# Kernel optimization log

Hardware: AMD Instinct MI355X
Metric: run time of the kernel (lower is better)

Reference implementation:

```python
import jax, jax.numpy as jnp
import numpy as np
from jax import lax


def _layernorm(x, scale, bias, eps=1e-5):
    m = x.mean(-1, keepdims=True)
    v = x.var(-1, keepdims=True)
    return (x - m) / jnp.sqrt(v + eps) * scale + bias


def setup_inputs() -> dict:
    key = jax.random.key(0)
    d = 21                      # code distance
    S = d * d - 1               # 440 tokens
    g = d + 1                   # 22x22 grid
    D, H, F, L, B = 256, 8, 512, 6, 64
    ks = jax.random.split(key, 24)
    w = 0.02
    idx = np.arange(S)
    scatter_positions = jnp.asarray(np.stack([idx // g, idx % g], axis=1), dtype=jnp.int64)
    inp = {
        'x': jax.random.randint(ks[0], (B, S), 0, 2).astype(jnp.int64),
        'scatter_positions': scatter_positions,
        'event_emb': w * jax.random.normal(ks[1], (2, D), jnp.float32),
        'pos_x': w * jax.random.normal(ks[2], (2 * d + 1, D), jnp.float32),
        'pos_y': w * jax.random.normal(ks[3], (2 * d + 1, D), jnp.float32),
        'stab_emb': w * jax.random.normal(ks[4], (2, D), jnp.float32),
        'tok_x': jax.random.randint(ks[5], (S,), 0, 2 * d + 1).astype(jnp.int64),
        'tok_y': jax.random.randint(ks[6], (S,), 0, 2 * d + 1).astype(jnp.int64),
        'tok_stab': jax.random.randint(ks[7], (S,), 0, 2).astype(jnp.int64),
        'attn_bias': w * jax.random.normal(ks[8], (S, S), jnp.float32),
        'Wqkv': w * jax.random.normal(ks[9], (L, 3 * D, D), jnp.float32),
        'bqkv': jnp.zeros((L, 3 * D), jnp.float32),
        'Wo': w * jax.random.normal(ks[10], (L, D, D), jnp.float32),
        'bo': jnp.zeros((L, D), jnp.float32),
        'W1': w * jax.random.normal(ks[11], (L, F, D), jnp.float32),
        'b1': jnp.zeros((L, F), jnp.float32),
        'W2': w * jax.random.normal(ks[12], (L, D, F), jnp.float32),
        'b2': jnp.zeros((L, D), jnp.float32),
        'ln1_s': jnp.ones((L, D), jnp.float32),
        'ln1_b': jnp.zeros((L, D), jnp.float32),
        'ln2_s': jnp.ones((L, D), jnp.float32),
        'ln2_b': jnp.zeros((L, D), jnp.float32),
        'cw1': w * jax.random.normal(ks[13], (L, D, D // H, 3, 3), jnp.float32),
        'cb1': jnp.zeros((L, D), jnp.float32),
        'cw2': w * jax.random.normal(ks[14], (L, D, D // H, 3, 3), jnp.float32),
        'cb2': jnp.zeros((L, D), jnp.float32),
        'cw3': w * jax.random.normal(ks[15], (L, D, D // H, 3, 3), jnp.float32),
        'cb3': jnp.zeros((L, D), jnp.float32),
    }
    return inp


def _forward(x, scatter_positions, event_emb, pos_x, pos_y, stab_emb, tok_x, tok_y,
             tok_stab, attn_bias, Wqkv, bqkv, Wo, bo, W1, b1, W2, b2,
             ln1_s, ln1_b, ln2_s, ln2_b, cw1, cb1, cw2, cb2, cw3, cb3):
    B, S = x.shape
    D = event_emb.shape[1]
    L = Wqkv.shape[0]
    H = D // cw1.shape[2]           # groups = n_heads
    dh = D // H
    g = int(np.sqrt(S + 1)) + 1     # (d+1) grid side
    rows = scatter_positions[:, 0]
    cols = scatter_positions[:, 1]

    # 2D positional encoding gathers + event embedding
    pos = pos_x[tok_x] + pos_y[tok_y] + stab_emb[tok_stab]   # [S, D]
    h = event_emb[x] + pos[None]                             # [B, S, D]

    scale = 1.0 / np.sqrt(dh).astype(np.float32)

    def conv(xg, wgt, b, dil):
        y = lax.conv_general_dilated(
            xg, wgt, window_strides=(1, 1), padding=[(dil, dil), (dil, dil)],
            rhs_dilation=(dil, dil), feature_group_count=H,
            dimension_numbers=('NCHW', 'OIHW', 'NCHW'))
        return jax.nn.relu(y + b[None, :, None, None])

    for l in range(L):
        # --- bias-MHA: QK^T * scale + learned relative bias, softmax, V ---
        qkv = jnp.einsum('bsd,ed->bse', h, Wqkv[l]) + bqkv[l]
        q, k, v = jnp.split(qkv, 3, axis=-1)
        q = q.reshape(B, S, H, dh)
        k = k.reshape(B, S, H, dh)
        v = v.reshape(B, S, H, dh)
        scores = jnp.einsum('bqhd,bkhd->bhqk', q, k) * scale + attn_bias[None, None]
        p = jax.nn.softmax(scores, axis=-1)
        o = jnp.einsum('bhqk,bkhd->bqhd', p, v).reshape(B, S, D)
        a = jnp.einsum('bsd,ed->bse', o, Wo[l]) + bo[l]
        h = _layernorm(h + a, ln1_s[l], ln1_b[l])
        # --- FFN (post-norm, ReLU) ---
        ff = jax.nn.relu(jnp.einsum('bsd,fd->bsf', h, W1[l]) + b1[l])
        ff = jnp.einsum('bsf,df->bsd', ff, W2[l]) + b2[l]
        h = _layernorm(h + ff, ln2_s[l], ln2_b[l])
        # --- scatter to 2D grid, grouped dilated convs, collect back ---
        grid = jnp.zeros((B, g, g, D), h.dtype).at[:, rows, cols].set(h)
        xg = grid.transpose(0, 3, 1, 2)                       # NCHW
        xg = 0.5 * (xg + conv(xg, cw1[l], cb1[l], 1)
                       + conv(xg, cw2[l], cb2[l], 2)
                       + conv(xg, cw3[l], cb3[l], 3))
        h = xg.transpose(0, 2, 3, 1)[:, rows, cols]           # collect_from_2d
    return h


def reference(x, scatter_positions, event_emb, pos_x, pos_y, stab_emb, tok_x, tok_y,
              tok_stab, attn_bias, Wqkv, bqkv, Wo, bo, W1, b1, W2, b2,
              ln1_s, ln1_b, ln2_s, ln2_b, cw1, cb1, cw2, cb2, cw3, cb3):
    return _forward(x, scatter_positions, event_emb, pos_x, pos_y, stab_emb, tok_x,
                    tok_y, tok_stab, attn_bias, Wqkv, bqkv, Wo, bo, W1, b1, W2, b2,
                    ln1_s, ln1_b, ln2_s, ln2_b, cw1, cb1, cw2, cb2, cw3, cb3)
```

## Files before the change

### kernel.cpp

```cpp
#include <hip/hip_runtime.h>
#include <hip/hip_bf16.h>

#define NB 64
#define S 440
#define D 256
#define H 8
#define DH 32
#define F 512
#define NL 6
#define G 22
#define NT (NB*S)
#define QBLK 224
#define QT2 2
#define PADK 456
#define CSTR 40

typedef __hip_bfloat16 bf16;
typedef unsigned short u16;
typedef __bf16 bf16x8 __attribute__((ext_vector_type(8)));
typedef float f32x4 __attribute__((ext_vector_type(4)));

#define MAGIC_BF16 0x3F803F80u

__device__ __align__(16) u16 g_abT[(S / 4) * S * 4];
#define WOFF_QKV 0
#define WOFF_WO  (NL*3*D*D)
#define WOFF_W1  (WOFF_WO + NL*D*D)
#define WOFF_W2  (WOFF_W1 + NL*F*D)
__device__ __align__(16) u16 g_wlin[WOFF_W2 + NL*D*F];
#define CVSTRIDE ((size_t)NL * 9 * 8 * 1024)
__device__ __align__(16) u16 g_cwt[3 * CVSTRIDE];
__device__ __align__(16) u16 g_qkvb[(size_t)NT * 768];
__device__ __align__(16) u16 g_obuf[(size_t)NT * D];
__device__ __align__(16) u16 g_acb [(size_t)NT * D];
__device__ __align__(16) u16 g_hbb [(size_t)NT * D];

static __device__ __forceinline__ float bf2f(bf16 x) { return __bfloat162float(x); }
static __device__ __forceinline__ float u2f(u16 u) {
  union { unsigned int i; float f; } t; t.i = ((unsigned int)u) << 16; return t.f;
}
static __device__ __forceinline__ float i2f(unsigned v) {
  union { unsigned u; float f; } t; t.u = v; return t.f;
}
static __device__ __forceinline__ u16 f2u(float f) {
  bf16 h = __float2bfloat16(f);
  return *(u16*)&h;
}
static __device__ __forceinline__ unsigned cvt_pk(float lo, float hi) {
  unsigned r;
  asm("v_cvt_pk_bf16_f32 %0, %1, %2" : "=v"(r) : "v"(lo), "v"(hi));
  return r;
}
static __device__ __forceinline__ float ldT(const void* p, size_t i, bool bfm) {
  return bfm ? u2f(((const u16*)p)[i]) : ((const float*)p)[i];
}
static __device__ __forceinline__ bf16x8 as_bf16x8(uint4 v) {
  union { uint4 u; bf16x8 b; } t; t.u = v; return t.b;
}
static __device__ __forceinline__ void gload_lds16(const u16* g, u16* l) {
  __builtin_amdgcn_global_load_lds(
      (const __attribute__((address_space(1))) void*)g,
      (__attribute__((address_space(3))) void*)l, 16, 0, 0);
}
static __device__ __forceinline__ const u16* selbuf(const void* ext, int sel) {
  return sel == 0 ? (const u16*)ext : sel == 1 ? g_hbb : sel == 2 ? g_qkvb : g_obuf;
}

__global__ void __launch_bounds__(256) cvt_conv(
    const void* __restrict__ src, int which, const unsigned* __restrict__ probe)
{
  bool bfm = (*probe == MAGIC_BF16);
  int n = NL * D * DH * 9;
  int i = blockIdx.x * 256 + threadIdx.x;
  if (i >= n) return;
  int kk = i % 9;
  int ic = (i / 9) % DH;
  int oc = (i / 288) % D;
  int l  = i / 73728;
  int g = oc >> 5, oc32 = oc & 31;
  u16 v;
  if (bfm) v = ((const u16*)src)[i];
  else     v = f2u(((const float*)src)[i]);
  g_cwt[(size_t)which * CVSTRIDE + (((size_t)l * 9 + kk) * 8 + g) * 1024 + oc32 * 32 + ic] = v;
}

__global__ void __launch_bounds__(256) cvt_lin(
    const void* __restrict__ src, size_t dstoff, int n,
    const unsigned* __restrict__ probe)
{
  bool bfm = (*probe == MAGIC_BF16);
  int i = blockIdx.x * 256 + threadIdx.x;
  if (i >= n) return;
  g_wlin[dstoff + i] = bfm ? ((const u16*)src)[i] : f2u(((const float*)src)[i]);
}

__global__ void __launch_bounds__(256) cvt_bias(
    const void* __restrict__ ab, const unsigned* __restrict__ probe)
{
  bool bfm = (*probe == MAGIC_BF16);
  int i = blockIdx.x * 256 + threadIdx.x;
  if (i >= (S / 4) * S * 4) return;
  int j = i & 3;
  int t = i >> 2;
  int q = t % S;
  int k4 = t / S;
  int k = k4 * 4 + j;
  float v = ldT(ab, (size_t)q * S + k, bfm) * 1.4426950408889634f;
  g_abT[i] = f2u(v);
}

__global__ void __launch_bounds__(256) embed_kernel(
    const int* __restrict__ x, const void* __restrict__ event_emb,
    const void* __restrict__ pos_x, const void* __restrict__ pos_y,
    const void* __restrict__ stab_emb, const int* __restrict__ tok_x,
    const int* __restrict__ tok_y, const int* __restrict__ tok_stab,
    bf16* __restrict__ h, const unsigned* __restrict__ probe)
{
  bool bfm = (*probe == MAGIC_BF16);
  int d = threadIdx.x;
#pragma unroll
  for (int r = 0; r < 4; ++r) {
    int t = blockIdx.x * 4 + r;
    int b = t / S, s = t - b * S;
    float v = ldT(event_emb, (size_t)x[b * S + s] * D + d, bfm)
            + ldT(pos_x, (size_t)tok_x[s] * D + d, bfm)
            + ldT(pos_y, (size_t)tok_y[s] * D + d, bfm)
            + ldT(stab_emb, (size_t)tok_stab[s] * D + d, bfm);
    h[(size_t)t * D + d] = __float2bfloat16(v);
  }
}

template <int RELU>
__global__ void __launch_bounds__(256) gemm_mfma(
    const void* __restrict__ Aext, int asel, size_t woff,
    const void* __restrict__ bias, size_t boff, int csel,
    int M, int N, int K, const unsigned* __restrict__ probe)
{
  bool bfm = (*probe == MAGIC_BF16);
  __shared__ u16 As[2][128][32];
  __shared__ u16 Ws[2][128][32];
  int tid = threadIdx.x;
  int bn = blockIdx.x, bm = blockIdx.y;
  int lane = tid & 63, w = tid >> 6;
  int wm = (w >> 1) * 64, wn = (w & 1) * 64;
  int qd = lane >> 4, ln16 = lane & 15;
  f32x4 zero4 = {0.f, 0.f, 0.f, 0.f};
  f32x4 acc[4][4];
#pragma unroll
  for (int i = 0; i < 4; ++i)
#pragma unroll
    for (int j = 0; j < 4; ++j) acc[i][j] = zero4;

  const u16* Au = selbuf(Aext, asel);
  u16* Cu = (csel == 0) ? g_qkvb : g_acb;
  const u16* Wu = g_wlin + woff;
  int srow = w * 32 + (lane >> 2);
  int skc  = (lane & 3) << 3;
  size_t abase = (size_t)(bm * 128 + srow) * K + skc;
  size_t wbase = (size_t)(bn * 128 + srow) * K + skc;

  gload_lds16(Au + abase,                   &As[0][w * 32][0]);
  gload_lds16(Au + abase + (size_t)16 * K,  &As[0][w * 32 + 16][0]);
  gload_lds16(Wu + wbase,                   &Ws[0][w * 32][0]);
  gload_lds16(Wu + wbase + (size_t)16 * K,  &Ws[0][w * 32 + 16][0]);

  int cur = 0;
  for (int k0 = 0; k0 < K; k0 += 32) {
    __syncthreads();
    if (k0 + 32 < K) {
      int nb = cur ^ 1;
      gload_lds16(Au + abase + k0 + 32,                  &As[nb][w * 32][0]);
      gload_lds16(Au + abase + (size_t)16 * K + k0 + 32, &As[nb][w * 32 + 16][0]);
      gload_lds16(Wu + wbase + k0 + 32,                  &Ws[nb][w * 32][0]);
      gload_lds16(Wu + wbase + (size_t)16 * K + k0 + 32, &Ws[nb][w * 32 + 16][0]);
    }
    bf16x8 af[4], bfr[4];
#pragma unroll
    for (int t = 0; t < 4; ++t) {
      af[t]  = *(const bf16x8*)&As[cur][wm + t * 16 + ln16][qd * 8];
      bfr[t] = *(const bf16x8*)&Ws[cur][wn + t * 16 + ln16][qd * 8];
    }
#pragma unroll
    for (int mt = 0; mt < 4; ++mt)
#pragma unroll
      for (int nt = 0; nt < 4; ++nt)
        acc[mt][nt] = __builtin_amdgcn_mfma_f32_16x16x32_bf16(af[mt], bfr[nt], acc[mt][nt], 0, 0, 0);
    cur ^= 1;
  }
#pragma unroll
  for (int nt = 0; nt < 4; ++nt) {
    int gcol = bn * 128 + wn + nt * 16 + ln16;
    float bv = ldT(bias, boff + gcol, bfm);
#pragma unroll
    for (int mt = 0; mt < 4; ++mt) {
#pragma unroll
      for (int r = 0; r < 4; ++r) {
        int grow = bm * 128 + wm + mt * 16 + qd * 4 + r;
        float v = acc[mt][nt][r] + bv;
        if (RELU) v = fmaxf(v, 0.f);
        Cu[(size_t)grow * N + gcol] = f2u(v);
      }
    }
  }
}

__global__ void __launch_bounds__(448) attn_mfma()
{
  __shared__ u16 VT[32 * PADK];
  int tid = threadIdx.x;
  int blk = blockIdx.x;
  int qt = (blk >> 3) & 1;
  int bh = ((blk >> 4) << 3) | (blk & 7);
  int hh = bh % H;
  int b  = bh / H;
  int lane = tid & 63, w = tid >> 6;
  int qd = lane >> 4, ln16 = lane & 15;
  const u16* qkvu = g_qkvb;

  unsigned* VT32 = (unsigned*)VT;
#pragma unroll
  for (int i = 0; i < 2; ++i) {
    int slot = tid + i * 448;
    int rp = slot >> 2, kc = slot & 3;
    int r0 = rp * 2;
    uint4 va = make_uint4(0, 0, 0, 0), vb = make_uint4(0, 0, 0, 0);
    if (r0 < S)     va = *(const uint4*)&qkvu[((size_t)(b * S + r0)) * 768 + 512 + hh * DH + kc * 8];
    if (r0 + 1 < S) vb = *(const uint4*)&qkvu[((size_t)(b * S + r0 + 1)) * 768 + 512 + hh * DH + kc * 8];
    unsigned aw[4] = {va.x, va.y, va.z, va.w};
    unsigned bw[4] = {vb.x, vb.y, vb.z, vb.w};
#pragma unroll
    for (int jj = 0; jj < 4; ++jj) {
      int d = kc * 8 + jj * 2;
      VT32[(size_t)(d    ) * (PADK / 2) + rp] = (aw[jj] & 0xffffu) | ((bw[jj] & 0xffffu) << 16);
      VT32[(size_t)(d + 1) * (PADK / 2) + rp] = (aw[jj] >> 16)     | ((bw[jj] >> 16) << 16);
    }
  }

  int q0 = qt * QBLK + w * 32;
  int qaA = q0 + ln16;      if (qaA >= S) qaA = S - 1;
  int qaB = q0 + 16 + ln16; if (qaB >= S) qaB = S - 1;
  bf16x8 afA = *(const bf16x8*)&qkvu[((size_t)(b * S + qaA)) * 768 + hh * DH + qd * 8];
  bf16x8 afB = *(const bf16x8*)&qkvu[((size_t)(b * S + qaB)) * 768 + hh * DH + qd * 8];
  __syncthreads();

  int kperm = ((ln16 >> 2) << 3) + (ln16 & 3);
  auto kload = [&](int ks_, int half) -> uint4 {
    int tok = ks_ * 32 + kperm + half * 4;
    if (tok >= S) tok = S - 1;
    return *(const uint4*)&qkvu[((size_t)(b * S + tok)) * 768 + 256 + hh * DH + qd * 8];
  };
  uint4 kn0 = kload(0, 0), kn1 = kload(0, 1);

  float lsA = 0.f, lsB = 0.f;
  f32x4 zero4 = {0.f, 0.f, 0.f, 0.f};
  f32x4 oa0A = zero4, oa1A = zero4;
  f32x4 oa0B = zero4, oa1B = zero4;
  const float SC2 = 0.17677669529663689f * 1.4426950408889634f;

  auto bias4 = [&](uint2 wv, float* o) {
    o[0] = i2f(wv.x << 16); o[1] = i2f(wv.x & 0xffff0000u);
    o[2] = i2f(wv.y << 16); o[3] = i2f(wv.y & 0xffff0000u);
  };

  auto body = [&](int ks, bool masked) {
    int k4a = ks * 8 + 2 * qd;
    int k4b = k4a + 1;
    if (masked) { if (k4a > 109) k4a = 109; if (k4b > 109) k4b = 109; }
    uint2 bwaA = *(const uint2*)&g_abT[((size_t)k4a * S + qaA) * 4];
    uint2 bwbA = *(const uint2*)&g_abT[((size_t)k4b * S + qaA) * 4];
    uint2 bwaB = *(const uint2*)&g_abT[((size_t)k4a * S + qaB) * 4];
    uint2 bwbB = *(const uint2*)&g_abT[((size_t)k4b * S + qaB) * 4];
    bf16x8 kf0 = as_bf16x8(kn0), kf1 = as_bf16x8(kn1);
    if (!masked) { kn0 = kload(ks + 1, 0); kn1 = kload(ks + 1, 1); }
    f32x4 s0A = __builtin_amdgcn_mfma_f32_16x16x32_bf16(kf0, afA, zero4, 0, 0, 0);
    f32x4 s1A = __builtin_amdgcn_mfma_f32_16x16x32_bf16(kf1, afA, zero4, 0, 0, 0);
    f32x4 s0B = __builtin_amdgcn_mfma_f32_16x16x32_bf16(kf0, afB, zero4, 0, 0, 0);
    f32x4 s1B = __builtin_amdgcn_mfma_f32_16x16x32_bf16(kf1, afB, zero4, 0, 0, 0);
    float bAA[4], bBA[4], bAB[4], bBB[4];
    bias4(bwaA, bAA); bias4(bwbA, bBA); bias4(bwaB, bAB); bias4(bwbB, bBB);
    float pA[8], pB[8];
    if (!masked) {
#pragma unroll
      for (int r = 0; r < 4; ++r) {
        pA[r]     = exp2f(fminf(fmaf(s0A[r], SC2, bAA[r]), 80.f));
        pA[4 + r] = exp2f(fminf(fmaf(s1A[r], SC2, bBA[r]), 80.f));
        pB[r]     = exp2f(fminf(fmaf(s0B[r], SC2, bAB[r]), 80.f));
        pB[4 + r] = exp2f(fminf(fmaf(s1B[r], SC2, bBB[r]), 80.f));
      }
    } else {
      int c0 = ks * 32 + qd * 8;
#pragma unroll
      for (int r = 0; r < 4; ++r) {
        bool m0 = (c0 + r < S), m1 = (c0 + 4 + r < S);
        pA[r]     = exp2f(m0 ? fminf(fmaf(s0A[r], SC2, bAA[r]), 80.f) : -1e30f);
        pA[4 + r] = exp2f(m1 ? fminf(fmaf(s1A[r], SC2, bBA[r]), 80.f) : -1e30f);
        pB[r]     = exp2f(m0 ? fminf(fmaf(s0B[r], SC2, bAB[r]), 80.f) : -1e30f);
        pB[4 + r] = exp2f(m1 ? fminf(fmaf(s1B[r], SC2, bBB[r]), 80.f) : -1e30f);
      }
    }
    lsA += ((pA[0] + pA[1]) + (pA[2] + pA[3])) + ((pA[4] + pA[5]) + (pA[6] + pA[7]));
    lsB += ((pB[0] + pB[1]) + (pB[2] + pB[3])) + ((pB[4] + pB[5]) + (pB[6] + pB[7]));
    bf16x8 pfA = as_bf16x8(make_uint4(
        cvt_pk(pA[0], pA[1]), cvt_pk(pA[2], pA[3]),
        cvt_pk(pA[4], pA[5]), cvt_pk(pA[6], pA[7])));
    bf16x8 pfB = as_bf16x8(make_uint4(
        cvt_pk(pB[0], pB[1]), cvt_pk(pB[2], pB[3]),
        cvt_pk(pB[4], pB[5]), cvt_pk(pB[6], pB[7])));
    int kb = ks * 32;
    bf16x8 vf0 = *(const bf16x8*)&VT[(size_t)ln16 * PADK + kb + qd * 8];
    bf16x8 vf1 = *(const bf16x8*)&VT[(size_t)(16 + ln16) * PADK + kb + qd * 8];
    oa0A = __builtin_amdgcn_mfma_f32_16x16x32_bf16(vf0, pfA, oa0A, 0, 0, 0);
    oa1A = __builtin_amdgcn_mfma_f32_16x16x32_bf16(vf1, pfA, oa1A, 0, 0, 0);
    oa0B = __builtin_amdgcn_mfma_f32_16x16x32_bf16(vf0, pfB, oa0B, 0, 0, 0);
    oa1B = __builtin_amdgcn_mfma_f32_16x16x32_bf16(vf1, pfB, oa1B, 0, 0, 0);
  };

  for (int ks = 0; ks < 13; ++ks) body(ks, false);
  body(13, true);

  lsA += __shfl_xor(lsA, 16, 64);
  lsA += __shfl_xor(lsA, 32, 64);
  lsB += __shfl_xor(lsB, 16, 64);
  lsB += __shfl_xor(lsB, 32, 64);
  float invA = 1.0f / lsA, invB = 1.0f / lsB;
  int qA = q0 + ln16, qB = q0 + 16 + ln16;
  if (qA < S) {
    u16* op = g_obuf + ((size_t)(b * S + qA)) * D + hh * DH;
    *(uint2*)&op[qd * 4] = make_uint2(
        cvt_pk(oa0A[0] * invA, oa0A[1] * invA),
        cvt_pk(oa0A[2] * invA, oa0A[3] * invA));
    *(uint2*)&op[16 + qd * 4] = make_uint2(
        cvt_pk(oa1A[0] * invA, oa1A[1] * invA),
        cvt_pk(oa1A[2] * invA, oa1A[3] * invA));
  }
  if (qB < S) {
    u16* op = g_obuf + ((size_t)(b * S + qB)) * D + hh * DH;
    *(uint2*)&op[qd * 4] = make_uint2(
        cvt_pk(oa0B[0] * invB, oa0B[1] * invB),
        cvt_pk(oa0B[2] * invB, oa0B[3] * invB));
    *(uint2*)&op[16 + qd * 4] = make_uint2(
        cvt_pk(oa1B[0] * invB, oa1B[1] * invB),
        cvt_pk(oa1B[2] * invB, oa1B[3] * invB));
  }
}

__global__ void __launch_bounds__(256) add_ln_kernel(
    void* __restrict__ hext, int hsel,
    const void* __restrict__ sc, size_t soff,
    const void* __restrict__ bi, size_t boff2,
    const unsigned* __restrict__ probe)
{
  bool bfm = (*probe == MAGIC_BF16);
  int wv = threadIdx.x >> 6, lane = threadIdx.x & 63;
  size_t row = (size_t)blockIdx.x * 4 + wv;
  u16* hp = (hsel ? g_hbb : (u16*)hext) + row * D;
  const u16* ap = g_acb + row * D;
  uint2 hv = *(const uint2*)&hp[lane * 4];
  uint2 av = *(const uint2*)&ap[lane * 4];
  float v0 = u2f((u16)(hv.x & 0xffffu)) + u2f((u16)(av.x & 0xffffu));
  float v1 = u2f((u16)(hv.x >> 16))     + u2f((u16)(av.x >> 16));
  float v2 = u2f((u16)(hv.y & 0xffffu)) + u2f((u16)(av.y & 0xffffu));
  float v3 = u2f((u16)(hv.y >> 16))     + u2f((u16)(av.y >> 16));
  float s = (v0 + v1) + (v2 + v3);
#pragma unroll
  for (int o = 1; o <= 32; o <<= 1) s += __shfl_xor(s, o, 64);
  float mean = s * (1.0f / D);
  float c0 = v0 - mean, c1 = v1 - mean, c2 = v2 - mean, c3 = v3 - mean;
  float vs = (c0 * c0 + c1 * c1) + (c2 * c2 + c3 * c3);
#pragma unroll
  for (int o = 1; o <= 32; o <<= 1) vs += __shfl_xor(vs, o, 64);
  float r = rsqrtf(vs * (1.0f / D) + 1e-5f);
  int d = lane * 4;
  float o0 = c0 * r * ldT(sc, soff + d,     bfm) + ldT(bi, boff2 + d,     bfm);
  float o1 = c1 * r * ldT(sc, soff + d + 1, bfm) + ldT(bi, boff2 + d + 1, bfm);
  float o2 = c2 * r * ldT(sc, soff + d + 2, bfm) + ldT(bi, boff2 + d + 2, bfm);
  float o3 = c3 * r * ldT(sc, soff + d + 3, bfm) + ldT(bi, boff2 + d + 3, bfm);
  *(uint2*)&hp[lane * 4] = make_uint2(cvt_pk(o0, o1), cvt_pk(o2, o3));
}

__global__ void __launch_bounds__(256) conv_mfma(
    const void* __restrict__ hin_ext, int hinsel,
    const void* __restrict__ cb1, const void* __restrict__ cb2,
    const void* __restrict__ cb3, size_t cboff,
    void* __restrict__ hout_ext, int houtsel, int l, int final_,
    const unsigned* __restrict__ probe)
{
  bool bfm = (*probe == MAGIC_BF16);
  __shared__ u16 X[17 * 28 * CSTR];
  int half = blockIdx.x, g = blockIdx.y, b = blockIdx.z;
  int tid = threadIdx.x;
  int rb = half ? 7 : -3;
  const u16* hin = selbuf(hin_ext, hinsel);

  for (int i = tid; i < 17 * 28 * CSTR / 8; i += 256)
    *(uint4*)&X[i * 8] = make_uint4(0, 0, 0, 0);
  __syncthreads();
  int rv0 = half ? 7 : 0;
  int nrow = half ? 13 : 14;
  for (int i = tid; i < nrow * 22 * 4; i += 256) {
    int tk = i >> 2, ch = i & 3;
    int r = rv0 + tk / 22, c = tk % 22;
    uint4 v = *(const uint4*)&hin[((size_t)(b * S + r * 22 + c)) * D + g * 32 + ch * 8];
    *(uint4*)&X[(((r - rb) * 28) + (c + 3)) * CSTR + ch * 8] = v;
  }
  __syncthreads();

  int lane = tid & 63, w = tid >> 6;
  int qd = lane >> 4, ln16 = lane & 15;
  int nt = w & 1;
  int mq = w >> 1;
  int t_base = half * 224 + mq * 112;
  int oc_l = nt * 16 + ln16;

  int aoff[7];
#pragma unroll
  for (int mt = 0; mt < 7; ++mt) {
    int t = t_base + mt * 16 + ln16;
    if (t > S - 1) t = S - 1;
    int r = t / 22, c = t - r * 22;
    aoff[mt] = (((r - rb) * 28) + (c + 3)) * CSTR;
  }
  f32x4 fin[7];
#pragma unroll
  for (int mt = 0; mt < 7; ++mt) {
#pragma unroll
    for (int r4 = 0; r4 < 4; ++r4) {
      int t = t_base + mt * 16 + qd * 4 + r4;
      if (t > S - 1) t = S - 1;
      int r = t / 22, c = t - r * 22;
      fin[mt][r4] = u2f(X[(((r - rb) * 28) + (c + 3)) * CSTR + oc_l]);
    }
  }

  f32x4 zero4 = {0.f, 0.f, 0.f, 0.f};
  const void* cbs[3] = {cb1, cb2, cb3};
#pragma unroll
  for (int cv = 0; cv < 3; ++cv) {
    int dil = cv + 1;
    f32x4 acc[7];
#pragma unroll
    for (int mt = 0; mt < 7; ++mt) acc[mt] = zero4;
    const u16* wt = g_cwt + ((size_t)cv * NL + l) * (9 * 8 * 1024);
#pragma unroll
    for (int kk = 0; kk < 9; ++kk) {
      int off = ((kk / 3 - 1) * 28 + (kk % 3 - 1)) * dil * CSTR;
      bf16x8 bfrag = *(const bf16x8*)&wt[((size_t)kk * 8 + g) * 1024 + oc_l * 32 + qd * 8];
#pragma unroll
      for (int mt = 0; mt < 7; ++mt) {
        bf16x8 a = *(const bf16x8*)&X[aoff[mt] + off + qd * 8];
        acc[mt] = __builtin_amdgcn_mfma_f32_16x16x32_bf16(a, bfrag, acc[mt], 0, 0, 0);
      }
    }
    float bv = ldT(cbs[cv], cboff + g * 32 + oc_l, bfm);
#pragma unroll
    for (int mt = 0; mt < 7; ++mt)
#pragma unroll
      for (int r4 = 0; r4 < 4; ++r4)
        fin[mt][r4] += fmaxf(acc[mt][r4] + bv, 0.f);
  }

#pragma unroll
  for (int mt = 0; mt < 7; ++mt)
#pragma unroll
    for (int r4 = 0; r4 < 4; ++r4) {
      int t = t_base + mt * 16 + qd * 4 + r4;
      if (t < S) {
        float outv = 0.5f * fin[mt][r4];
        size_t oi = ((size_t)(b * S + t)) * D + g * 32 + oc_l;
        if (final_ && !bfm) ((float*)hout_ext)[oi] = outv;
        else {
          u16* ho = houtsel ? g_hbb : (u16*)hout_ext;
          ho[oi] = f2u(outv);
        }
      }
    }
}

extern "C" void kernel_launch(void* const* d_in, const int* in_sizes, int n_in,
                              void* d_out, int out_size, void* d_ws, size_t ws_size,
                              hipStream_t stream)
{
  const int*  x         = (const int*)d_in[0];
  const void* event_emb = d_in[2];
  const void* pos_x     = d_in[3];
  const void* pos_y     = d_in[4];
  const void* stab_emb  = d_in[5];
  const int*  tok_x     = (const int*)d_in[6];
  const int*  tok_y     = (const int*)d_in[7];
  const int*  tok_stab  = (const int*)d_in[8];
  const void* attn_bias = d_in[9];
  const void* Wqkv      = d_in[10];
  const void* bqkv      = d_in[11];
  const void* Wo        = d_in[12];
  const void* bo        = d_in[13];
  const void* W1        = d_in[14];
  const void* b1        = d_in[15];
  const void* W2        = d_in[16];
  const void* b2        = d_in[17];
  const void* ln1_s     = d_in[18];
  const void* ln1_b     = d_in[19];
  const void* ln2_s     = d_in[20];
  const void* ln2_b     = d_in[21];
  const void* cw1       = d_in[22];
  const void* cb1       = d_in[23];
  const void* cw2       = d_in[24];
  const void* cb2       = d_in[25];
  const void* cw3       = d_in[26];
  const void* cb3       = d_in[27];
  (void)in_sizes; (void)n_in; (void)out_size; (void)d_ws; (void)ws_size;
  const unsigned* probe = (const unsigned*)ln1_s;

  int ncv = NL * D * DH * 9;
  cvt_conv<<<(ncv + 255)/256, 256, 0, stream>>>(cw1, 0, probe);
  cvt_conv<<<(ncv + 255)/256, 256, 0, stream>>>(cw2, 1, probe);
  cvt_conv<<<(ncv + 255)/256, 256, 0, stream>>>(cw3, 2, probe);
  cvt_bias<<<((S/4)*S*4 + 255)/256, 256, 0, stream>>>(attn_bias, probe);
  cvt_lin<<<(NL*3*D*D + 255)/256, 256, 0, stream>>>(Wqkv, WOFF_QKV, NL*3*D*D, probe);
  cvt_lin<<<(NL*D*D   + 255)/256, 256, 0, stream>>>(Wo,   WOFF_WO,  NL*D*D,   probe);
  cvt_lin<<<(NL*F*D   + 255)/256, 256, 0, stream>>>(W1,   WOFF_W1,  NL*F*D,   probe);
  cvt_lin<<<(NL*D*F   + 255)/256, 256, 0, stream>>>(W2,   WOFF_W2,  NL*D*F,   probe);

  bf16* hout_ = (bf16*)d_out;
  embed_kernel<<<NT/4, 256, 0, stream>>>(x, event_emb, pos_x, pos_y, stab_emb,
                                         tok_x, tok_y, tok_stab, hout_, probe);

  for (int l = 0; l < NL; ++l) {
    int hs = l & 1;
    int fin = (l == NL - 1) ? 1 : 0;
    gemm_mfma<0><<<dim3(6, NT/128), 256, 0, stream>>>(
        hout_, hs, (size_t)WOFF_QKV + (size_t)l*3*D*D, bqkv, (size_t)l*3*D, 0,
        NT, 3*D, D, probe);
    attn_mfma<<<NB*H*QT2, 448, 0, stream>>>();
    gemm_mfma<0><<<dim3(2, NT/128), 256, 0, stream>>>(
        hout_, 3, (size_t)WOFF_WO + (size_t)l*D*D, bo, (size_t)l*D, 1,
        NT, D, D, probe);
    add_ln_kernel<<<NT/4, 256, 0, stream>>>(hout_, hs, ln1_s, (size_t)l*D, ln1_b, (size_t)l*D, probe);
    gemm_mfma<1><<<dim3(4, NT/128), 256, 0, stream>>>(
        hout_, hs, (size_t)WOFF_W1 + (size_t)l*F*D, b1, (size_t)l*F, 0,
        NT, F, D, probe);
    gemm_mfma<0><<<dim3(2, NT/128), 256, 0, stream>>>(
        hout_, 2, (size_t)WOFF_W2 + (size_t)l*D*F, b2, (size_t)l*D, 1,
        NT, D, F, probe);
    add_ln_kernel<<<NT/4, 256, 0, stream>>>(hout_, hs, ln2_s, (size_t)l*D, ln2_b, (size_t)l*D, probe);
    conv_mfma<<<dim3(2, 8, NB), 256, 0, stream>>>(
        hout_, hs, cb1, cb2, cb3, (size_t)l*D, hout_, hs ^ 1, l, fin, probe);
  }
}
```

Measured before the change: 1.422 ms.

## Fuse output-projection and FFN-down GEMMs with residual add and LayerNorm

Adds a gemm_ln kernel in which each block computes a full 128x256 output row tile, adds bias and the residual, and applies LayerNorm using a cross-wave reduction through shared memory. It replaces the Wo and W2 GEMMs plus their separate add_ln kernels, removing the bf16 round trip of the intermediate activations and two launches per layer. Grid parallelism drops from 2x220 blocks to 220 larger blocks of 512 threads. Variance is now computed as E[x^2]-mean^2, which is less numerically stable than the previous two-pass form.

```diff
diff --git a/kernel.cpp b/kernel.cpp
--- a/kernel.cpp
+++ b/kernel.cpp
@@ -202,6 +202,125 @@
       }
     }
   }
+}
+
+__global__ void __launch_bounds__(512) gemm_ln(
+    const void* __restrict__ Aext, int asel, size_t woff,
+    const void* __restrict__ bias, size_t boff,
+    void* __restrict__ hext, int hsel,
+    const void* __restrict__ sc, size_t soff,
+    const void* __restrict__ bi, size_t boff2,
+    int K, const unsigned* __restrict__ probe)
+{
+  bool bfm = (*probe == MAGIC_BF16);
+  __shared__ u16 As[2][128][32];
+  __shared__ u16 Ws[2][256][32];
+  __shared__ float redS[4][128];
+  __shared__ float redQ[4][128];
+  int tid = threadIdx.x;
+  int bm = blockIdx.x;
+  int lane = tid & 63, w = tid >> 6;
+  int wm = (w >> 2) * 64, wn = (w & 3) * 64;
+  int qd = lane >> 4, ln16 = lane & 15;
+  f32x4 zero4 = {0.f, 0.f, 0.f, 0.f};
+  f32x4 acc[4][4];
+#pragma unroll
+  for (int i = 0; i < 4; ++i)
+#pragma unroll
+    for (int j = 0; j < 4; ++j) acc[i][j] = zero4;
+
+  const u16* Au = selbuf(Aext, asel);
+  u16* hp = hsel ? g_hbb : (u16*)hext;
+  const u16* Wu = g_wlin + woff;
+  int arow = w * 16 + (lane >> 2);
+  int wrow = w * 32 + (lane >> 2);
+  int skc  = (lane & 3) << 3;
+  size_t abase = (size_t)(bm * 128 + arow) * K + skc;
+  size_t wbase = (size_t)wrow * K + skc;
+
+  gload_lds16(Au + abase,                  &As[0][w * 16][0]);
+  gload_lds16(Wu + wbase,                  &Ws[0][w * 32][0]);
+  gload_lds16(Wu + wbase + (size_t)16 * K, &Ws[0][w * 32 + 16][0]);
+
+  int cur = 0;
+  for (int k0 = 0; k0 < K; k0 += 32) {
+    __syncthreads();
+    if (k0 + 32 < K) {
+      int nb = cur ^ 1;
+      gload_lds16(Au + abase + k0 + 32,                  &As[nb][w * 16][0]);
+      gload_lds16(Wu + wbase + k0 + 32,                  &Ws[nb][w * 32][0]);
+      gload_lds16(Wu + wbase + (size_t)16 * K + k0 + 32, &Ws[nb][w * 32 + 16][0]);
+    }
+    bf16x8 af[4], bfr[4];
+#pragma unroll
+    for (int t = 0; t < 4; ++t) {
+      af[t]  = *(const bf16x8*)&As[cur][wm + t * 16 + ln16][qd * 8];
+      bfr[t] = *(const bf16x8*)&Ws[cur][wn + t * 16 + ln16][qd * 8];
+    }
+#pragma unroll
+    for (int mt = 0; mt < 4; ++mt)
+#pragma unroll
+      for (int nt = 0; nt < 4; ++nt)
+        acc[mt][nt] = __builtin_amdgcn_mfma_f32_16x16x32_bf16(af[mt], bfr[nt], acc[mt][nt], 0, 0, 0);
+    cur ^= 1;
+  }
+
+  float bv[4];
+#pragma unroll
+  for (int nt = 0; nt < 4; ++nt) bv[nt] = ldT(bias, boff + wn + nt * 16 + ln16, bfm);
+#pragma unroll
+  for (int mt = 0; mt < 4; ++mt)
+#pragma unroll
+    for (int r = 0; r < 4; ++r) {
+      size_t grow = (size_t)bm * 128 + wm + mt * 16 + qd * 4 + r;
+#pragma unroll
+      for (int nt = 0; nt < 4; ++nt) {
+        int col = wn + nt * 16 + ln16;
+        acc[mt][nt][r] += bv[nt] + u2f(hp[grow * D + col]);
+      }
+    }
+#pragma unroll
+  for (int mt = 0; mt < 4; ++mt)
+#pragma unroll
+    for (int r = 0; r < 4; ++r) {
+      float s = (acc[mt][0][r] + acc[mt][1][r]) + (acc[mt][2][r] + acc[mt][3][r]);
+      float q = (acc[mt][0][r] * acc[mt][0][r] + acc[mt][1][r] * acc[mt][1][r])
+              + (acc[mt][2][r] * acc[mt][2][r] + acc[mt][3][r] * acc[mt][3][r]);
+#pragma unroll
+      for (int m = 1; m <= 8; m <<= 1) {
+        s += __shfl_xor(s, m, 64);
+        q += __shfl_xor(q, m, 64);
+      }
+      if (ln16 == 0) {
+        int lrow = wm + mt * 16 + qd * 4 + r;
+        redS[w & 3][lrow] = s;
+        redQ[w & 3][lrow] = q;
+      }
+    }
+  __syncthreads();
+  float ls[4], lb[4];
+#pragma unroll
+  for (int nt = 0; nt < 4; ++nt) {
+    ls[nt] = ldT(sc, soff + wn + nt * 16 + ln16, bfm);
+    lb[nt] = ldT(bi, boff2 + wn + nt * 16 + ln16, bfm);
+  }
+#pragma unroll
+  for (int mt = 0; mt < 4; ++mt)
+#pragma unroll
+    for (int r = 0; r < 4; ++r) {
+      int lrow = wm + mt * 16 + qd * 4 + r;
+      float Ssum = (redS[0][lrow] + redS[1][lrow]) + (redS[2][lrow] + redS[3][lrow]);
+      float Qsum = (redQ[0][lrow] + redQ[1][lrow]) + (redQ[2][lrow] + redQ[3][lrow]);
+      float mean = Ssum * (1.0f / D);
+      float rstd = rsqrtf(Qsum * (1.0f / D) - mean * mean + 1e-5f);
+      size_t grow = (size_t)bm * 128 + lrow;
+#pragma unroll
+      for (int nt = 0; nt < 4; ++nt) {
+        int col = wn + nt * 16 + ln16;
+        float o = (acc[mt][nt][r] - mean) * rstd * ls[nt] + lb[nt];
+        hp[grow * D + col] = f2u(o);
+      }
+    }
 }
 
 __global__ void __launch_bounds__(448) attn_mfma()
@@ -342,40 +461,6 @@
         cvt_pk(oa1B[0] * invB, oa1B[1] * invB),
         cvt_pk(oa1B[2] * invB, oa1B[3] * invB));
   }
-}
-
-__global__ void __launch_bounds__(256) add_ln_kernel(
-    void* __restrict__ hext, int hsel,
-    const void* __restrict__ sc, size_t soff,
-    const void* __restrict__ bi, size_t boff2,
-    const unsigned* __restrict__ probe)
-{
-  bool bfm = (*probe == MAGIC_BF16);
-  int wv = threadIdx.x >> 6, lane = threadIdx.x & 63;
-  size_t row = (size_t)blockIdx.x * 4 + wv;
-  u16* hp = (hsel ? g_hbb : (u16*)hext) + row * D;
-  const u16* ap = g_acb + row * D;
-  uint2 hv = *(const uint2*)&hp[lane * 4];
-  uint2 av = *(const uint2*)&ap[lane * 4];
-  float v0 = u2f((u16)(hv.x & 0xffffu)) + u2f((u16)(av.x & 0xffffu));
-  float v1 = u2f((u16)(hv.x >> 16))     + u2f((u16)(av.x >> 16));
-  float v2 = u2f((u16)(hv.y & 0xffffu)) + u2f((u16)(av.y & 0xffffu));
-  float v3 = u2f((u16)(hv.y >> 16))     + u2f((u16)(av.y >> 16));
-  float s = (v0 + v1) + (v2 + v3);
-#pragma unroll
-  for (int o = 1; o <= 32; o <<= 1) s += __shfl_xor(s, o, 64);
-  float mean = s * (1.0f / D);
-  float c0 = v0 - mean, c1 = v1 - mean, c2 = v2 - mean, c3 = v3 - mean;
-  float vs = (c0 * c0 + c1 * c1) + (c2 * c2 + c3 * c3);
-#pragma unroll
-  for (int o = 1; o <= 32; o <<= 1) vs += __shfl_xor(vs, o, 64);
-  float r = rsqrtf(vs * (1.0f / D) + 1e-5f);
-  int d = lane * 4;
-  float o0 = c0 * r * ldT(sc, soff + d,     bfm) + ldT(bi, boff2 + d,     bfm);
-  float o1 = c1 * r * ldT(sc, soff + d + 1, bfm) + ldT(bi, boff2 + d + 1, bfm);
-  float o2 = c2 * r * ldT(sc, soff + d + 2, bfm) + ldT(bi, boff2 + d + 2, bfm);
-  float o3 = c3 * r * ldT(sc, soff + d + 3, bfm) + ldT(bi, boff2 + d + 3, bfm);
-  *(uint2*)&hp[lane * 4] = make_uint2(cvt_pk(o0, o1), cvt_pk(o2, o3));
 }
 
 __global__ void __launch_bounds__(256) conv_mfma(
@@ -531,17 +616,15 @@
         hout_, hs, (size_t)WOFF_QKV + (size_t)l*3*D*D, bqkv, (size_t)l*3*D, 0,
         NT, 3*D, D, probe);
     attn_mfma<<<NB*H*QT2, 448, 0, stream>>>();
-    gemm_mfma<0><<<dim3(2, NT/128), 256, 0, stream>>>(
-        hout_, 3, (size_t)WOFF_WO + (size_t)l*D*D, bo, (size_t)l*D, 1,
-        NT, D, D, probe);
-    add_ln_kernel<<<NT/4, 256, 0, stream>>>(hout_, hs, ln1_s, (size_t)l*D, ln1_b, (size_t)l*D, probe);
+    gemm_ln<<<NT/128, 512, 0, stream>>>(
+        hout_, 3, (size_t)WOFF_WO + (size_t)l*D*D, bo, (size_t)l*D,
+        hout_, hs, ln1_s, (size_t)l*D, ln1_b, (size_t)l*D, D, probe);
     gemm_mfma<1><<<dim3(4, NT/128), 256, 0, stream>>>(
         hout_, hs, (size_t)WOFF_W1 + (size_t)l*F*D, b1, (size_t)l*F, 0,
         NT, F, D, probe);
-    gemm_mfma<0><<<dim3(2, NT/128), 256, 0, stream>>>(
-        hout_, 2, (size_t)WOFF_W2 + (size_t)l*D*F, b2, (size_t)l*D, 1,
-        NT, D, F, probe);
-    add_ln_kernel<<<NT/4, 256, 0, stream>>>(hout_, hs, ln2_s, (size_t)l*D, ln2_b, (size_t)l*D, probe);
+    gemm_ln<<<NT/128, 512, 0, stream>>>(
+        hout_, 2, (size_t)WOFF_W2 + (size_t)l*D*F, b2, (size_t)l*D,
+        hout_, hs, ln2_s, (size_t)l*D, ln2_b, (size_t)l*D, F, probe);
     conv_mfma<<<dim3(2, 8, NB), 256, 0, stream>>>(
         hout_, hs, cb1, cb2, cb3, (size_t)l*D, hout_, hs ^ 1, l, fin, probe);
   }
```

Measured after the change: 1.264 ms. 11.1% less time.
